# Kernel optimization log

Hardware: AMD Instinct MI355X
Metric: run time of the kernel (lower is better)

The kernel has to match this reference:

```python
import jax, jax.numpy as jnp
import numpy as np

H = 512
W = 512


def setup_inputs() -> dict:
    key = jax.random.key(0)
    k1, k2 = jax.random.split(key)
    batch_images = jax.random.normal(k1, (4, 3, H, W), dtype=jnp.float32)
    # (B, N, 2) float label coordinates (x, y) in [0, H)
    batch_labels = jax.random.uniform(k2, (4, 64, 2), dtype=jnp.float32) * H
    sigma = jnp.float32(4.0)  # learned nn.Parameter
    return {"batch_images": batch_images, "batch_labels": batch_labels, "sigma": sigma}


def reference(batch_images, batch_labels, sigma):
    # Original: for each label (x,y), build full HxW gaussian
    #   exp(-((x_grid - x)^2 + (y_grid - y)^2) / (2 sigma^2)),
    # normalize by its own sum, accumulate into density[b, 0].
    # The 2-D gaussian is separable: g2d = gy (outer) gx and
    # sum(g2d) = sum(gy) * sum(gx), so the accumulation over labels is a
    # single einsum with no (B,N,H,W) intermediate.
    B = batch_images.shape[0]
    Hh = batch_images.shape[2]
    Ww = batch_images.shape[3]
    xs = jnp.arange(Ww, dtype=batch_labels.dtype)  # x varies along last axis
    ys = jnp.arange(Hh, dtype=batch_labels.dtype)  # y varies along row axis
    lx = batch_labels[..., 0]  # (B, N)
    ly = batch_labels[..., 1]  # (B, N)
    inv = 1.0 / (2.0 * sigma * sigma)
    gx = jnp.exp(-((xs[None, None, :] - lx[..., None]) ** 2) * inv)  # (B, N, W)
    gy = jnp.exp(-((ys[None, None, :] - ly[..., None]) ** 2) * inv)  # (B, N, H)
    gx = gx / jnp.sum(gx, axis=-1, keepdims=True)
    gy = gy / jnp.sum(gy, axis=-1, keepdims=True)
    density = jnp.einsum("bnh,bnw->bhw", gy, gx)  # sum over labels
    return density[:, None, :, :]  # (B, 1, H, W)
```

## Files before the change

### kernel.cpp

```cpp
#include <hip/hip_runtime.h>

#define BB 4
#define NN 64
#define HH 512
#define WW 512
#define RPB 8
#define LOG2E 1.4426950408889634f
#define CUT 18.0f

__global__ __launch_bounds__(512) void fused_density_kernel(
    const float* __restrict__ labels,
    const float* __restrict__ sigma,
    float* __restrict__ out)
{
    const int b    = blockIdx.x / (HH / RPB);
    const int y0   = (blockIdx.x % (HH / RPB)) * RPB;
    const int t    = threadIdx.x;
    const int wave = t >> 6;
    const int lane = t & 63;

    __shared__ float lx_s[NN];
    __shared__ float ly_s[NN];
    __shared__ float w_s[NN];
    __shared__ float eyw_s[NN][RPB];
    __shared__ int   cnt_s;

    const float s    = sigma[0];
    const float c2   = -LOG2E / (2.0f * s * s);
    const float rad  = __builtin_sqrtf(CUT / (-c2));

    if (wave == 0) {
        const float lx = labels[(b * NN + lane) * 2 + 0];
        const float ly = labels[(b * NN + lane) * 2 + 1];
        const float dlo  = (float)y0 - ly;
        const float dhi  = ly - (float)(y0 + RPB - 1);
        const float dmin = fmaxf(fmaxf(dlo, dhi), 0.0f);
        const bool keep  = dmin < rad;
        const unsigned long long mask = __ballot(keep);
        if (keep) {
            const int idx = __popcll(mask & ((1ULL << lane) - 1ULL));
            lx_s[idx] = lx;
            ly_s[idx] = ly;
        }
        if (lane == 0) cnt_s = (int)__popcll(mask);
    }
    __syncthreads();
    const int cnt = cnt_s;

    for (int j = wave; j < cnt; j += 8) {
        const float lx = lx_s[j], ly = ly_s[j];
        float sx = 0.0f, sy = 0.0f;
#pragma unroll
        for (int k = 0; k < WW; k += 64) {
            const float v  = (float)(lane + k);
            const float dx = v - lx;
            const float dy = v - ly;
            sx += __builtin_amdgcn_exp2f(c2 * dx * dx);
            sy += __builtin_amdgcn_exp2f(c2 * dy * dy);
        }
#pragma unroll
        for (int off = 32; off > 0; off >>= 1) {
            sx += __shfl_xor(sx, off, 64);
            sy += __shfl_xor(sy, off, 64);
        }
        if (lane == 0) w_s[j] = 1.0f / (sx * sy);
    }
    __syncthreads();

    if (t < cnt * RPB) {
        const int j = t >> 3, r = t & (RPB - 1);
        const float dy = (float)(y0 + r) - ly_s[j];
        eyw_s[j][r] = __builtin_amdgcn_exp2f(c2 * dy * dy) * w_s[j];
    }
    __syncthreads();

    float acc[RPB];
#pragma unroll
    for (int r = 0; r < RPB; ++r) acc[r] = 0.0f;
    const float xf = (float)t;
    for (int j = 0; j < cnt; ++j) {
        const float dx = xf - lx_s[j];
        const float ex = __builtin_amdgcn_exp2f(c2 * dx * dx);
#pragma unroll
        for (int r = 0; r < RPB; ++r)
            acc[r] = fmaf(ex, eyw_s[j][r], acc[r]);
    }
#pragma unroll
    for (int r = 0; r < RPB; ++r)
        out[(b * HH + y0 + r) * WW + t] = acc[r];
}

extern "C" void kernel_launch(void* const* d_in, const int* in_sizes, int n_in,
                              void* d_out, int out_size, void* d_ws, size_t ws_size,
                              hipStream_t stream) {
    const float* labels = (const float*)d_in[1];
    const float* sigma  = (const float*)d_in[2];
    float*       out    = (float*)d_out;

    fused_density_kernel<<<BB * (HH / RPB), 512, 0, stream>>>(labels, sigma, out);
}
```

Before: 9.692 us.

## Replace per-label gaussian sum loops with closed-form erfc tail approximation

Each label's gaussian normalization sum over the 512 grid points is now computed analytically: the integral of the gaussian minus two boundary tail terms, using an Abramowitz-Stegun erfc polynomial plus a correction term. This removes the wave-parallel summation loop, its shuffle reduction and two barriers, and folds the row-gaussian precompute into the label-filtering step. Rows per block also drop from 8 to 4, doubling the block count. The analytic sum is an approximation, so accuracy depends on sigma and the tolerance, and more blocks recompute the x-direction exponentials more often.

```diff
diff --git a/kernel.cpp b/kernel.cpp
--- a/kernel.cpp
+++ b/kernel.cpp
@@ -4,83 +4,82 @@
 #define NN 64
 #define HH 512
 #define WW 512
-#define RPB 8
+#define RPB 4
 #define LOG2E 1.4426950408889634f
 #define CUT 18.0f
+
+__device__ __forceinline__ float exp2f_fast(float x) { return __builtin_amdgcn_exp2f(x); }
+
+__device__ __forceinline__ float tail_T(float u, float A, float invs2,
+                                        float c2, float i24) {
+    const float g  = exp2f_fast(c2 * u * u);
+    const float x  = u * invs2;
+    const float ax = fabsf(x);
+    const float t  = 1.0f / fmaf(0.3275911f, ax, 1.0f);
+    const float poly = t * fmaf(t, fmaf(t, fmaf(t, fmaf(t, 1.061405429f,
+                        -1.453152027f), 1.421413741f), -0.284496736f),
+                        0.254829592f);
+    const float e    = poly * g;
+    const float erfc = (x >= 0.0f) ? e : (2.0f - e);
+    return fmaf(A, erfc, -i24 * u * g);
+}
 
 __global__ __launch_bounds__(512) void fused_density_kernel(
     const float* __restrict__ labels,
     const float* __restrict__ sigma,
     float* __restrict__ out)
 {
-    const int b    = blockIdx.x / (HH / RPB);
-    const int y0   = (blockIdx.x % (HH / RPB)) * RPB;
-    const int t    = threadIdx.x;
-    const int wave = t >> 6;
-    const int lane = t & 63;
+    const int nrb = HH / RPB;
+    const int b   = blockIdx.x / nrb;
+    const int y0  = (blockIdx.x % nrb) * RPB;
+    const int t   = threadIdx.x;
 
     __shared__ float lx_s[NN];
-    __shared__ float ly_s[NN];
-    __shared__ float w_s[NN];
     __shared__ float eyw_s[NN][RPB];
     __shared__ int   cnt_s;
 
-    const float s    = sigma[0];
-    const float c2   = -LOG2E / (2.0f * s * s);
-    const float rad  = __builtin_sqrtf(CUT / (-c2));
+    const float s  = sigma[0];
+    const float c2 = -LOG2E / (2.0f * s * s);
 
-    if (wave == 0) {
-        const float lx = labels[(b * NN + lane) * 2 + 0];
-        const float ly = labels[(b * NN + lane) * 2 + 1];
+    if (t < NN) {
+        const float lx = labels[(b * NN + t) * 2 + 0];
+        const float ly = labels[(b * NN + t) * 2 + 1];
+        const float rad = __builtin_sqrtf(CUT / (-c2));
         const float dlo  = (float)y0 - ly;
         const float dhi  = ly - (float)(y0 + RPB - 1);
         const float dmin = fmaxf(fmaxf(dlo, dhi), 0.0f);
-        const bool keep  = dmin < rad;
+        const bool  keep = dmin < rad;
         const unsigned long long mask = __ballot(keep);
         if (keep) {
-            const int idx = __popcll(mask & ((1ULL << lane) - 1ULL));
+            const int idx = __popcll(mask & ((1ULL << t) - 1ULL));
+            const float A     = s * 1.2533141373155003f;
+            const float Bf    = s * 2.5066282746310002f;
+            const float invs2 = 1.0f / (s * 1.4142135623730951f);
+            const float i24   = 1.0f / (24.0f * s * s);
+            const float Sx = Bf - tail_T(lx + 0.5f, A, invs2, c2, i24)
+                                - tail_T((float)(WW - 1) + 0.5f - lx, A, invs2, c2, i24);
+            const float Sy = Bf - tail_T(ly + 0.5f, A, invs2, c2, i24)
+                                - tail_T((float)(HH - 1) + 0.5f - ly, A, invs2, c2, i24);
+            const float w  = 1.0f / (Sx * Sy);
             lx_s[idx] = lx;
-            ly_s[idx] = ly;
+#pragma unroll
+            for (int r = 0; r < RPB; ++r) {
+                const float dy = (float)(y0 + r) - ly;
+                eyw_s[idx][r] = exp2f_fast(c2 * dy * dy) * w;
+            }
         }
-        if (lane == 0) cnt_s = (int)__popcll(mask);
-    }
-    __syncthreads();
-    const int cnt = cnt_s;
-
-    for (int j = wave; j < cnt; j += 8) {
-        const float lx = lx_s[j], ly = ly_s[j];
-        float sx = 0.0f, sy = 0.0f;
-#pragma unroll
-        for (int k = 0; k < WW; k += 64) {
-            const float v  = (float)(lane + k);
-            const float dx = v - lx;
-            const float dy = v - ly;
-            sx += __builtin_amdgcn_exp2f(c2 * dx * dx);
-            sy += __builtin_amdgcn_exp2f(c2 * dy * dy);
-        }
-#pragma unroll
-        for (int off = 32; off > 0; off >>= 1) {
-            sx += __shfl_xor(sx, off, 64);
-            sy += __shfl_xor(sy, off, 64);
-        }
-        if (lane == 0) w_s[j] = 1.0f / (sx * sy);
+        if (t == 0) cnt_s = (int)__popcll(mask);
     }
     __syncthreads();
 
-    if (t < cnt * RPB) {
-        const int j = t >> 3, r = t & (RPB - 1);
-        const float dy = (float)(y0 + r) - ly_s[j];
-        eyw_s[j][r] = __builtin_amdgcn_exp2f(c2 * dy * dy) * w_s[j];
-    }
-    __syncthreads();
-
+    const int   cnt = cnt_s;
+    const float xf  = (float)t;
     float acc[RPB];
 #pragma unroll
     for (int r = 0; r < RPB; ++r) acc[r] = 0.0f;
-    const float xf = (float)t;
     for (int j = 0; j < cnt; ++j) {
         const float dx = xf - lx_s[j];
-        const float ex = __builtin_amdgcn_exp2f(c2 * dx * dx);
+        const float ex = exp2f_fast(c2 * dx * dx);
 #pragma unroll
         for (int r = 0; r < RPB; ++r)
             acc[r] = fmaf(ex, eyw_s[j][r], acc[r]);
```

After: 9.791 us. No clear change (+1.0%).
